# Optimization experiments

Measured on AMD Instinct MI355X. Metric: run time of the kernel, lower is better.

## Reference

```python
import jax, jax.numpy as jnp
import numpy as np

N = 100_000          # nodes
E = 3_200_000        # edges (avg degree 32)
DIMS = [6, 20, 15, 10, 5, 2]


def setup_inputs() -> dict:
    key = jax.random.key(0)
    ks = jax.random.split(key, 3 + 2 * 5)
    inp = {
        "x": jax.random.normal(ks[0], (N, DIMS[0]), jnp.float32),
        "edge_index": jax.random.randint(ks[1], (2, E), 0, N, jnp.int32),
        "edge_weight": jax.random.uniform(ks[2], (E,), jnp.float32),
    }
    for i in range(5):
        din, dout = DIMS[i], DIMS[i + 1]
        s = 1.0 / np.sqrt(din)
        inp[f"w_rel{i}"] = jax.random.normal(ks[3 + 2 * i], (din, dout), jnp.float32) * s
        inp[f"b_rel{i}"] = jnp.zeros((dout,), jnp.float32)
        inp[f"w_root{i}"] = jax.random.normal(ks[4 + 2 * i], (din, dout), jnp.float32) * s
    return inp


def _graph_conv(x, src, dst, w, W_rel, b_rel, W_root):
    # PyG GraphConv: lin_rel(scatter_add(w_e * x_src)) + lin_root(x)
    msg = x[src] * w[:, None]                                  # [E, din]
    agg = jax.ops.segment_sum(msg, dst, num_segments=N)        # [N, din]
    return agg @ W_rel + b_rel + x @ W_root                    # [N, dout]


def reference(x, edge_index, edge_weight,
              w_rel0, b_rel0, w_root0,
              w_rel1, b_rel1, w_root1,
              w_rel2, b_rel2, w_root2,
              w_rel3, b_rel3, w_root3,
              w_rel4, b_rel4, w_root4):
    src, dst = edge_index[0], edge_index[1]
    layers = [
        (w_rel0, b_rel0, w_root0),
        (w_rel1, b_rel1, w_root1),
        (w_rel2, b_rel2, w_root2),
        (w_rel3, b_rel3, w_root3),
        (w_rel4, b_rel4, w_root4),
    ]
    for W_rel, b_rel, W_root in layers:
        x = jax.nn.relu(_graph_conv(x, src, dst, edge_weight, W_rel, b_rel, W_root))
    return jax.nn.softmax(x, axis=1)
```

## Files before the change

### kernel.cpp

```cpp
#include <hip/hip_runtime.h>
#include <hip/hip_fp16.h>
#include <stdint.h>

#define N_NODES 100000
#define N_EDGES 3200000
#define BN      128
#define NB      782
#define NCH_H   1024
#define CH_H    (N_EDGES / NCH_H)
#define CPL     (NCH_H / 64)
#define PAD_PER 98
#define NCH_S   512
#define CH_S    (N_EDGES / NCH_S)
#define FPS     (NCH_H / NCH_S)
#define BS1     1024
#define S1_IT   ((CH_S + BS1 - 1) / BS1)
#define BS2     512
#define S2_CAP  4608
#define R2IT    9
#define BLOCK   256
#define W_SCALE 32767.0f
#define W_INV   (1.0f / 32767.0f)

__global__ void hist_kernel(const int* __restrict__ dst, int* __restrict__ hist_g,
                            const float* __restrict__ x, __half* __restrict__ xpad) {
    __shared__ int h[NB];
    for (int b = threadIdx.x; b < NB; b += BLOCK) h[b] = 0;
    {
        int i = blockIdx.x * PAD_PER + threadIdx.x;
        if (threadIdx.x < PAD_PER && i < N_NODES) {
            const float* xr = x + (size_t)i * 6;
            __half2 hh[4];
            hh[0] = __halves2half2(__float2half(xr[0]), __float2half(xr[1]));
            hh[1] = __halves2half2(__float2half(xr[2]), __float2half(xr[3]));
            hh[2] = __halves2half2(__float2half(xr[4]), __float2half(xr[5]));
            hh[3] = __halves2half2(__float2half(0.f),   __float2half(0.f));
            *(uint4*)(xpad + (size_t)i * 8) = *(uint4*)hh;
        }
    }
    __syncthreads();
    const int c  = blockIdx.x;
    const int k0 = c * CH_H;
    for (int k = threadIdx.x; k < CH_H; k += BLOCK)
        atomicAdd(&h[dst[k0 + k] >> 7], 1);
    __syncthreads();
    for (int b = threadIdx.x; b < NB; b += BLOCK)
        hist_g[c * NB + b] = h[b];
}

__global__ void reduce_kernel(const int* __restrict__ hist_g, int* __restrict__ tot) {
    int w    = (blockIdx.x * blockDim.x + threadIdx.x) >> 6;
    int lane = threadIdx.x & 63;
    if (w >= NB) return;
    int ls = 0;
    const int cbase = lane * CPL;
    #pragma unroll
    for (int i = 0; i < CPL; ++i) ls += hist_g[(cbase + i) * NB + w];
    #pragma unroll
    for (int d = 32; d >= 1; d >>= 1) ls += __shfl_xor(ls, d);
    if (lane == 0) tot[w] = ls;
}

#define SCAN_T   1024
__global__ void scan_kernel(const int* __restrict__ cnt, int* __restrict__ bstart,
                            int* __restrict__ gcur) {
    __shared__ int part[SCAN_T];
    int t = threadIdx.x;
    int v = (t < NB) ? cnt[t] : 0;
    part[t] = v;
    __syncthreads();
    for (int off = 1; off < SCAN_T; off <<= 1) {
        int u = (t >= off) ? part[t - off] : 0;
        __syncthreads();
        part[t] += u;
        __syncthreads();
    }
    if (t < NB) { int e = part[t] - v; bstart[t] = e; gcur[t] = e; }
}

__global__ void __launch_bounds__(BS1)
scatter1_kernel(const int* __restrict__ src, const int* __restrict__ dst,
                const float* __restrict__ w,
                int* __restrict__ gcur,
                const int* __restrict__ hist_g,
                uint2* __restrict__ rec1) {
    __shared__ uint2 stage[CH_S];
    __shared__ int h[NB];
    __shared__ int delta[NB];
    __shared__ int wtot[BS1 / 64];

    const int c  = blockIdx.x;
    const int k0 = c * CH_S;
    const int t  = threadIdx.x;

    int      dv[S1_IT];
    uint32_t sv[S1_IT];
    float    wv[S1_IT];
    #pragma unroll
    for (int i = 0; i < S1_IT; ++i) {
        int k = t + i * BS1;
        if (k < CH_S) {
            dv[i] = dst[k0 + k];
            sv[i] = (uint32_t)src[k0 + k];
            wv[i] = w[k0 + k];
        }
    }

    for (int b = t; b < NB; b += BS1) {
        int s = 0;
        #pragma unroll
        for (int f = 0; f < FPS; ++f)
            s += hist_g[(size_t)(FPS * c + f) * NB + b];
        h[b] = s;
    }
    __syncthreads();

    {
        const int base = t * 2;
        int v[2], ls = 0;
        #pragma unroll
        for (int i = 0; i < 2; ++i) {
            int idx = base + i;
            v[i] = (idx < NB) ? h[idx] : 0;
            ls += v[i];
        }
        int lane = t & 63, wvi = t >> 6;
        int run = ls;
        #pragma unroll
        for (int d = 1; d < 64; d <<= 1) {
            int u = __shfl_up(run, d);
            if (lane >= d) run += u;
        }
        if (lane == 63) wtot[wvi] = run;
        __syncthreads();
        int wexcl = 0;
        for (int i = 0; i < wvi; ++i) wexcl += wtot[i];
        int excl = wexcl + run - ls;
        #pragma unroll
        for (int i = 0; i < 2; ++i) {
            int idx = base + i;
            if (idx < NB) {
                int gb = atomicAdd(&gcur[idx], v[i]);
                h[idx]     = excl;
                delta[idx] = gb - excl;
                excl += v[i];
            }
        }
    }
    __syncthreads();

    #pragma unroll
    for (int i = 0; i < S1_IT; ++i) {
        int k = t + i * BS1;
        if (k < CH_S) {
            int d = dv[i];
            int b = d >> 7;
            int pos = atomicAdd(&h[b], 1);
            uint32_t w15 = (uint32_t)__float2uint_rn(wv[i] * W_SCALE);
            uint2 r;
            r.x = sv[i] | ((uint32_t)(d & 127) << 17);
            r.y = w15 | ((uint32_t)b << 15);
            stage[pos] = r;
        }
    }
    __syncthreads();

    #pragma unroll
    for (int i = 0; i < S1_IT; ++i) {
        int k = t + i * BS1;
        if (k < CH_S) {
            uint2 r = stage[k];
            int b = (int)(r.y >> 15);
            rec1[delta[b] + k] = r;
        }
    }
}

__global__ void __launch_bounds__(BS2)
scatter2_kernel(const uint2* __restrict__ rec1,
                const int* __restrict__ bstart, const int* __restrict__ tot,
                uint32_t* __restrict__ rec2,
                int2* __restrict__ rowcnt) {
    __shared__ int h[BN];
    __shared__ int cur[BN];
    __shared__ int wtot2[2];
    __shared__ uint32_t stage[S2_CAP];
    const int b  = blockIdx.x;
    const int s0 = bstart[b];
    const int n  = tot[b];
    const int t  = threadIdx.x;
    if (t < BN) h[t] = 0;
    __syncthreads();

    uint2 rv[R2IT];
    #pragma unroll
    for (int i = 0; i < R2IT; ++i) {
        int k = t + i * BS2;
        uint2 r = (k < n) ? rec1[s0 + k] : make_uint2(0u, 0u);
        rv[i] = r;
        if (k < n) atomicAdd(&h[r.x >> 17], 1);
    }
    for (int k = t + R2IT * BS2; k < n; k += BS2)
        atomicAdd(&h[rec1[s0 + k].x >> 17], 1);
    __syncthreads();

    int v = 0, run = 0;
    if (t < BN) {
        v = h[t];
        run = v;
        int lane = t & 63;
        #pragma unroll
        for (int d = 1; d < 64; d <<= 1) {
            int u = __shfl_up(run, d);
            if (lane >= d) run += u;
        }
        if (lane == 63) wtot2[t >> 6] = run;
    }
    __syncthreads();
    if (t < BN) {
        int excl = run - v + ((t >= 64) ? wtot2[0] : 0);
        cur[t] = excl;
        int node = b * BN + t;
        if (node < N_NODES) rowcnt[node] = make_int2(s0 + excl, v);
    }
    __syncthreads();

    #pragma unroll
    for (int i = 0; i < R2IT; ++i) {
        int k = t + i * BS2;
        if (k < n) {
            uint2 r = rv[i];
            int dl = (int)(r.x >> 17);
            uint32_t r2 = (r.x & 0x1FFFF) | ((r.y & 0x7FFF) << 17);
            int pos = atomicAdd(&cur[dl], 1);
            if (pos < S2_CAP) stage[pos] = r2;
            else              rec2[s0 + pos] = r2;
        }
    }
    for (int k = t + R2IT * BS2; k < n; k += BS2) {
        uint2 r = rec1[s0 + k];
        int dl = (int)(r.x >> 17);
        uint32_t r2 = (r.x & 0x1FFFF) | ((r.y & 0x7FFF) << 17);
        int pos = atomicAdd(&cur[dl], 1);
        if (pos < S2_CAP) stage[pos] = r2;
        else              rec2[s0 + pos] = r2;
    }
    __syncthreads();
    for (int i = t; i < n && i < S2_CAP; i += BS2)
        rec2[s0 + i] = stage[i];
}

__global__ void layer0_kernel(const __half* __restrict__ xpad,
                              const uint32_t* __restrict__ rec,
                              const int2* __restrict__ rowcnt,
                              const float* __restrict__ wrel0, const float* __restrict__ brel0,
                              const float* __restrict__ wroot0,
                              const float* __restrict__ wrel1, const float* __restrict__ brel1,
                              const float* __restrict__ wroot1,
                              __half* __restrict__ pn, float* __restrict__ oinitn) {
    __shared__ float s_wrel0[6 * 20], s_wroot0[6 * 20], s_b0[20];
    __shared__ float s_wrel1[20 * 15], s_wroot1[20 * 15], s_b1[15];
    for (int t = threadIdx.x; t < 120; t += BLOCK) {
        s_wrel0[t]  = wrel0[t];
        s_wroot0[t] = wroot0[t];
    }
    for (int t = threadIdx.x; t < 300; t += BLOCK) {
        s_wrel1[t]  = wrel1[t];
        s_wroot1[t] = wroot1[t];
    }
    if (threadIdx.x < 20) s_b0[threadIdx.x] = brel0[threadIdx.x];
    if (threadIdx.x < 15) s_b1[threadIdx.x] = brel1[threadIdx.x];
    __syncthreads();

    int t = blockIdx.x * blockDim.x + threadIdx.x;
    int node = t >> 3;
    int q    = t & 7;

    float agg[6] = {0.f, 0.f, 0.f, 0.f, 0.f, 0.f};
    const int2 rc = rowcnt[node];
    const int s = rc.x;
    const int e = rc.x + rc.y;
    for (int k = s + q; k < e; k += 32) {
        uint32_t rv[4];
        float    wv[4];
        #pragma unroll
        for (int u = 0; u < 4; ++u) {
            int kk = k + 8 * u;
            rv[u] = (kk < e) ? rec[kk] : 0u;
            wv[u] = (float)(rv[u] >> 17) * W_INV;
        }
        uint4 raw[4];
        #pragma unroll
        for (int u = 0; u < 4; ++u)
            raw[u] = *(const uint4*)(xpad + (size_t)(rv[u] & 0x1FFFF) * 8);
        #pragma unroll
        for (int u = 0; u < 4; ++u) {
            const __half2* h = (const __half2*)&raw[u];
            float w = wv[u];
            agg[0] += w * __low2float(h[0]);  agg[1] += w * __high2float(h[0]);
            agg[2] += w * __low2float(h[1]);  agg[3] += w * __high2float(h[1]);
            agg[4] += w * __low2float(h[2]);  agg[5] += w * __high2float(h[2]);
        }
    }
    #pragma unroll
    for (int i = 0; i < 6; ++i) {
        agg[i] += __shfl_xor(agg[i], 1);
        agg[i] += __shfl_xor(agg[i], 2);
        agg[i] += __shfl_xor(agg[i], 4);
    }
    uint4 raws = *(const uint4*)(xpad + (size_t)node * 8);
    const __half2* hs = (const __half2*)&raws;
    float xv[6] = { __low2float(hs[0]), __high2float(hs[0]),
                    __low2float(hs[1]), __high2float(hs[1]),
                    __low2float(hs[2]), __high2float(hs[2]) };
    float ov[20];
    #pragma unroll
    for (int j = 0; j < 20; ++j) {
        float o = s_b0[j];
        #pragma unroll
        for (int i = 0; i < 6; ++i)
            o += agg[i] * s_wrel0[i * 20 + j] + xv[i] * s_wroot0[i * 20 + j];
        ov[j] = fmaxf(o, 0.f);
    }
    {
        float pk[2] = {0.f, 0.f};
        #pragma unroll
        for (int kk = 0; kk < 2; ++kk) {
            int k = 2 * q + kk;
            if (k < 15) {
                float sacc = 0.f;
                #pragma unroll
                for (int j = 0; j < 20; ++j) sacc += ov[j] * s_wrel1[j * 15 + k];
                pk[kk] = sacc;
            }
        }
        ((__half2*)(pn + (size_t)node * 16))[q] =
            __halves2half2(__float2half(pk[0]), __float2half(pk[1]));
    }
    #pragma unroll
    for (int kk = 0; kk < 2; ++kk) {
        int k = q + kk * 8;
        if (k < 15) {
            float sacc = s_b1[k];
            #pragma unroll
            for (int j = 0; j < 20; ++j) sacc += ov[j] * s_wroot1[j * 15 + k];
            oinitn[(size_t)node * 15 + k] = sacc;
        }
    }
}

template<int DOUT, int SPH, int NDOUT, int NSPH, bool LAST>
__global__ void gather_kernel(const __half* __restrict__ p, const float* __restrict__ oinit,
                              const uint32_t* __restrict__ rec,
                              const int2* __restrict__ rowcnt,
                              const float* __restrict__ wrel_n, const float* __restrict__ brel_n,
                              const float* __restrict__ wroot_n,
                              __half* __restrict__ pn, float* __restrict__ oinitn,
                              float* __restrict__ out) {
    __shared__ float s_wrel[LAST ? 1 : DOUT * NDOUT];
    __shared__ float s_wroot[LAST ? 1 : DOUT * NDOUT];
    __shared__ float s_b[LAST ? 1 : (NDOUT > 0 ? NDOUT : 1)];
    if constexpr (!LAST) {
        for (int t = threadIdx.x; t < DOUT * NDOUT; t += BLOCK) {
            s_wrel[t]  = wrel_n[t];
            s_wroot[t] = wroot_n[t];
        }
        if (threadIdx.x < NDOUT) s_b[threadIdx.x] = brel_n[threadIdx.x];
        __syncthreads();
    }

    int t = blockIdx.x * blockDim.x + threadIdx.x;
    int node = t >> 3;
    int q    = t & 7;

    float af[SPH];
    #pragma unroll
    for (int i = 0; i < SPH; ++i) af[i] = 0.f;

    const int2 rc = rowcnt[node];
    const int s = rc.x;
    const int e = rc.x + rc.y;
    constexpr int NR = (SPH >= 8) ? SPH / 8 : 1;
    for (int k = s + q; k < e; k += 32) {
        uint32_t rv[4];
        float    wv[4];
        #pragma unroll
        for (int u = 0; u < 4; ++u) {
            int kk = k + 8 * u;
            rv[u] = (kk < e) ? rec[kk] : 0u;
            wv[u] = (float)(rv[u] >> 17) * W_INV;
        }
        if constexpr (SPH >= 8) {
            uint4 raw[4 * NR];
            #pragma unroll
            for (int u = 0; u < 4; ++u) {
                const uint4* ps = (const uint4*)(p + (size_t)(rv[u] & 0x1FFFF) * SPH);
                #pragma unroll
                for (int v = 0; v < NR; ++v) raw[u * NR + v] = ps[v];
            }
            #pragma unroll
            for (int u = 0; u < 4; ++u) {
                float w = wv[u];
                #pragma unroll
                for (int v = 0; v < NR; ++v) {
                    const __half2* h = (const __half2*)&raw[u * NR + v];
                    #pragma unroll
                    for (int jj = 0; jj < 4; ++jj) {
                        af[v * 8 + 2 * jj]     += w * __low2float(h[jj]);
                        af[v * 8 + 2 * jj + 1] += w * __high2float(h[jj]);
                    }
                }
            }
        } else {
            uint32_t raw[4];
            #pragma unroll
            for (int u = 0; u < 4; ++u)
                raw[u] = *(const uint32_t*)(p + (size_t)(rv[u] & 0x1FFFF) * SPH);
            #pragma unroll
            for (int u = 0; u < 4; ++u) {
                __half2 h = *(const __half2*)&raw[u];
                af[0] += wv[u] * __low2float(h);
                af[1] += wv[u] * __high2float(h);
            }
        }
    }
    #pragma unroll
    for (int i = 0; i < SPH; ++i) {
        af[i] += __shfl_xor(af[i], 1);
        af[i] += __shfl_xor(af[i], 2);
        af[i] += __shfl_xor(af[i], 4);
    }

    if constexpr (LAST) {
        if (q == 0) {
            float o0 = af[0] + oinit[(size_t)node * 2 + 0];
            float o1 = af[1] + oinit[(size_t)node * 2 + 1];
            float m = fmaxf(o0, o1);
            float e0 = __expf(o0 - m), e1 = __expf(o1 - m);
            float inv = 1.f / (e0 + e1);
            out[(size_t)node * 2 + 0] = e0 * inv;
            out[(size_t)node * 2 + 1] = e1 * inv;
        }
    } else {
        float ov[DOUT];
        #pragma unroll
        for (int j = 0; j < DOUT; ++j)
            ov[j] = fmaxf(af[j] + oinit[(size_t)node * DOUT + j], 0.f);

        if (q < NSPH / 2) {
            float pk[2] = {0.f, 0.f};
            #pragma unroll
            for (int kk = 0; kk < 2; ++kk) {
                int k = 2 * q + kk;
                if (k < NDOUT) {
                    float sacc = 0.f;
                    #pragma unroll
                    for (int j = 0; j < DOUT; ++j) sacc += ov[j] * s_wrel[j * NDOUT + k];
                    pk[kk] = sacc;
                }
            }
            ((__half2*)(pn + (size_t)node * NSPH))[q] =
                __halves2half2(__float2half(pk[0]), __float2half(pk[1]));
        }
        #pragma unroll
        for (int kk = 0; kk < 2; ++kk) {
            int k = q + kk * 8;
            if (k < NDOUT) {
                float sacc = s_b[k];
                #pragma unroll
                for (int j = 0; j < DOUT; ++j) sacc += ov[j] * s_wroot[j * NDOUT + k];
                oinitn[(size_t)node * NDOUT + k] = sacc;
            }
        }
    }
}


extern "C" void kernel_launch(void* const* d_in, const int* in_sizes, int n_in,
                              void* d_out, int out_size, void* d_ws, size_t ws_size,
                              hipStream_t stream) {
    const float* x  = (const float*)d_in[0];
    const int*   ei = (const int*)d_in[1];
    const float* ew = (const float*)d_in[2];
    const float* wrel[5]  = { (const float*)d_in[3], (const float*)d_in[6],
                              (const float*)d_in[9], (const float*)d_in[12],
                              (const float*)d_in[15] };
    const float* brel[5]  = { (const float*)d_in[4], (const float*)d_in[7],
                              (const float*)d_in[10], (const float*)d_in[13],
                              (const float*)d_in[16] };
    const float* wroot[5] = { (const float*)d_in[5], (const float*)d_in[8],
                              (const float*)d_in[11], (const float*)d_in[14],
                              (const float*)d_in[17] };

    char* ws = (char*)d_ws;
    size_t off = 0;
    auto alloc = [&](size_t bytes) -> void* {
        void* ptr = ws + off;
        off += (bytes + 255) & ~(size_t)255;
        return ptr;
    };
    char*     regionA   = (char*)alloc((size_t)N_EDGES * 8);
    uint2*    rec1      = (uint2*)regionA;
    __half*   pA        = (__half*)regionA;
    __half*   pB        = (__half*)(regionA + (size_t)4  * 1024 * 1024);
    float*    oA        = (float*)(regionA + (size_t)8  * 1024 * 1024);
    float*    oB        = (float*)(regionA + (size_t)16 * 1024 * 1024);
    uint32_t* rec2      = (uint32_t*)alloc((size_t)N_EDGES * 4);
    __half*   xpad      = (__half*)alloc((size_t)N_NODES * 8 * 2);
    int*      hist_g    = (int*)alloc((size_t)NCH_H * NB * 4);
    int*      tot       = (int*)alloc((size_t)NB * 4);
    int*      bstart    = (int*)alloc((size_t)NB * 4);
    int*      gcur      = (int*)alloc((size_t)NB * 4);
    int2*     rowcnt    = (int2*)alloc((size_t)N_NODES * 8);

    const int* srcv = ei;
    const int* dstv = ei + N_EDGES;

    const int gN8 = (8 * N_NODES + BLOCK - 1) / BLOCK;

    hist_kernel    <<<NCH_H, BLOCK, 0, stream>>>(dstv, hist_g, x, xpad);
    reduce_kernel  <<<(NB + 3) / 4, BLOCK, 0, stream>>>(hist_g, tot);
    scan_kernel    <<<1, SCAN_T, 0, stream>>>(tot, bstart, gcur);
    scatter1_kernel<<<NCH_S, BS1, 0, stream>>>(srcv, dstv, ew, gcur, hist_g, rec1);
    scatter2_kernel<<<NB, BS2, 0, stream>>>(rec1, bstart, tot, rec2, rowcnt);

    layer0_kernel<<<gN8, BLOCK, 0, stream>>>(xpad, rec2, rowcnt,
                                             wrel[0], brel[0], wroot[0],
                                             wrel[1], brel[1], wroot[1], pA, oA);
    gather_kernel<15, 16, 10, 16, false><<<gN8, BLOCK, 0, stream>>>(
        pA, oA, rec2, rowcnt, wrel[2], brel[2], wroot[2], pB, oB, nullptr);
    gather_kernel<10, 16, 5, 8, false><<<gN8, BLOCK, 0, stream>>>(
        pB, oB, rec2, rowcnt, wrel[3], brel[3], wroot[3], pA, oA, nullptr);
    gather_kernel<5, 8, 2, 2, false><<<gN8, BLOCK, 0, stream>>>(
        pA, oA, rec2, rowcnt, wrel[4], brel[4], wroot[4], pB, oB, nullptr);
    gather_kernel<2, 2, 0, 0, true><<<gN8, BLOCK, 0, stream>>>(
        pB, oB, rec2, rowcnt, nullptr, nullptr, nullptr,
        nullptr, nullptr, (float*)d_out);
}
```

Baseline: 282.3 us.

## Replace two-level bucket sort CSR build with per-node atomic counting sort

Builds the destination-sorted edge list with a per-node histogram using global atomics, a two-pass block scan, and a direct atomic-slot scatter. This replaces the old bucketed two-stage scatter with its shared-memory staging. Node activation buffers now get dedicated allocations instead of aliasing the old record region. The new path spreads 3.2M global atomics over 100k counters and writes scattered 4-byte records, trading extra random global traffic for fewer passes. Edge order within each row also becomes nondeterministic.

```diff
diff --git a/kernel.cpp b/kernel.cpp
--- a/kernel.cpp
+++ b/kernel.cpp
@@ -4,31 +4,26 @@
 
 #define N_NODES 100000
 #define N_EDGES 3200000
-#define BN      128
-#define NB      782
-#define NCH_H   1024
-#define CH_H    (N_EDGES / NCH_H)
-#define CPL     (NCH_H / 64)
-#define PAD_PER 98
-#define NCH_S   512
-#define CH_S    (N_EDGES / NCH_S)
-#define FPS     (NCH_H / NCH_S)
-#define BS1     1024
-#define S1_IT   ((CH_S + BS1 - 1) / BS1)
-#define BS2     512
-#define S2_CAP  4608
-#define R2IT    9
 #define BLOCK   256
+#define GN8     3125
+#define NHB     782
+#define NSB     98
 #define W_SCALE 32767.0f
 #define W_INV   (1.0f / 32767.0f)
 
-__global__ void hist_kernel(const int* __restrict__ dst, int* __restrict__ hist_g,
-                            const float* __restrict__ x, __half* __restrict__ xpad) {
-    __shared__ int h[NB];
-    for (int b = threadIdx.x; b < NB; b += BLOCK) h[b] = 0;
+__global__ void __launch_bounds__(1024)
+zero_kernel(int* __restrict__ ncnt) {
+    int i = blockIdx.x * 1024 + threadIdx.x;
+    if (i < N_NODES) ncnt[i] = 0;
+}
+
+__global__ void __launch_bounds__(1024)
+nhist_kernel(const int* __restrict__ dst, int* __restrict__ ncnt,
+             const float* __restrict__ x, __half* __restrict__ xpad) {
+    const int t = threadIdx.x, blk = blockIdx.x;
     {
-        int i = blockIdx.x * PAD_PER + threadIdx.x;
-        if (threadIdx.x < PAD_PER && i < N_NODES) {
+        int i = blk * 128 + t;
+        if (t < 128 && i < N_NODES) {
             const float* xr = x + (size_t)i * 6;
             __half2 hh[4];
             hh[0] = __halves2half2(__float2half(xr[0]), __float2half(xr[1]));
@@ -38,216 +33,84 @@
             *(uint4*)(xpad + (size_t)i * 8) = *(uint4*)hh;
         }
     }
-    __syncthreads();
-    const int c  = blockIdx.x;
-    const int k0 = c * CH_H;
-    for (int k = threadIdx.x; k < CH_H; k += BLOCK)
-        atomicAdd(&h[dst[k0 + k] >> 7], 1);
-    __syncthreads();
-    for (int b = threadIdx.x; b < NB; b += BLOCK)
-        hist_g[c * NB + b] = h[b];
-}
-
-__global__ void reduce_kernel(const int* __restrict__ hist_g, int* __restrict__ tot) {
-    int w    = (blockIdx.x * blockDim.x + threadIdx.x) >> 6;
-    int lane = threadIdx.x & 63;
-    if (w >= NB) return;
-    int ls = 0;
-    const int cbase = lane * CPL;
-    #pragma unroll
-    for (int i = 0; i < CPL; ++i) ls += hist_g[(cbase + i) * NB + w];
-    #pragma unroll
-    for (int d = 32; d >= 1; d >>= 1) ls += __shfl_xor(ls, d);
-    if (lane == 0) tot[w] = ls;
-}
-
-#define SCAN_T   1024
-__global__ void scan_kernel(const int* __restrict__ cnt, int* __restrict__ bstart,
-                            int* __restrict__ gcur) {
-    __shared__ int part[SCAN_T];
-    int t = threadIdx.x;
-    int v = (t < NB) ? cnt[t] : 0;
+    const int base = blk * 4096 + t;
+    int dv[4];
+    #pragma unroll
+    for (int u = 0; u < 4; ++u) {
+        int k = base + u * 1024;
+        dv[u] = (k < N_EDGES) ? dst[k] : -1;
+    }
+    #pragma unroll
+    for (int u = 0; u < 4; ++u)
+        if (dv[u] >= 0) atomicAdd(&ncnt[dv[u]], 1);
+}
+
+__global__ void __launch_bounds__(1024)
+partial_kernel(const int* __restrict__ ncnt, int* __restrict__ nexcl,
+               int* __restrict__ ptot) {
+    __shared__ int part[1024];
+    const int t = threadIdx.x;
+    const int idx = blockIdx.x * 1024 + t;
+    int v = (idx < N_NODES) ? ncnt[idx] : 0;
     part[t] = v;
     __syncthreads();
-    for (int off = 1; off < SCAN_T; off <<= 1) {
+    for (int off = 1; off < 1024; off <<= 1) {
         int u = (t >= off) ? part[t - off] : 0;
         __syncthreads();
         part[t] += u;
         __syncthreads();
     }
-    if (t < NB) { int e = part[t] - v; bstart[t] = e; gcur[t] = e; }
-}
-
-__global__ void __launch_bounds__(BS1)
-scatter1_kernel(const int* __restrict__ src, const int* __restrict__ dst,
-                const float* __restrict__ w,
-                int* __restrict__ gcur,
-                const int* __restrict__ hist_g,
-                uint2* __restrict__ rec1) {
-    __shared__ uint2 stage[CH_S];
-    __shared__ int h[NB];
-    __shared__ int delta[NB];
-    __shared__ int wtot[BS1 / 64];
-
-    const int c  = blockIdx.x;
-    const int k0 = c * CH_S;
-    const int t  = threadIdx.x;
-
-    int      dv[S1_IT];
-    uint32_t sv[S1_IT];
-    float    wv[S1_IT];
-    #pragma unroll
-    for (int i = 0; i < S1_IT; ++i) {
-        int k = t + i * BS1;
-        if (k < CH_S) {
-            dv[i] = dst[k0 + k];
-            sv[i] = (uint32_t)src[k0 + k];
-            wv[i] = w[k0 + k];
-        }
-    }
-
-    for (int b = t; b < NB; b += BS1) {
-        int s = 0;
-        #pragma unroll
-        for (int f = 0; f < FPS; ++f)
-            s += hist_g[(size_t)(FPS * c + f) * NB + b];
-        h[b] = s;
-    }
+    if (idx < N_NODES) nexcl[idx] = part[t] - v;
+    if (t == 1023) ptot[blockIdx.x] = part[t];
+}
+
+__global__ void __launch_bounds__(1024)
+fixup_kernel(const int* __restrict__ ncnt, const int* __restrict__ nexcl,
+             const int* __restrict__ ptot,
+             int2* __restrict__ rowcnt, int* __restrict__ ncur) {
+    __shared__ int red[1024];
+    const int t = threadIdx.x, blk = blockIdx.x;
+    red[t] = (t < blk) ? ptot[t] : 0;
     __syncthreads();
-
-    {
-        const int base = t * 2;
-        int v[2], ls = 0;
-        #pragma unroll
-        for (int i = 0; i < 2; ++i) {
-            int idx = base + i;
-            v[i] = (idx < NB) ? h[idx] : 0;
-            ls += v[i];
-        }
-        int lane = t & 63, wvi = t >> 6;
-        int run = ls;
-        #pragma unroll
-        for (int d = 1; d < 64; d <<= 1) {
-            int u = __shfl_up(run, d);
-            if (lane >= d) run += u;
-        }
-        if (lane == 63) wtot[wvi] = run;
+    for (int off = 512; off >= 1; off >>= 1) {
+        if (t < off) red[t] += red[t + off];
         __syncthreads();
-        int wexcl = 0;
-        for (int i = 0; i < wvi; ++i) wexcl += wtot[i];
-        int excl = wexcl + run - ls;
-        #pragma unroll
-        for (int i = 0; i < 2; ++i) {
-            int idx = base + i;
-            if (idx < NB) {
-                int gb = atomicAdd(&gcur[idx], v[i]);
-                h[idx]     = excl;
-                delta[idx] = gb - excl;
-                excl += v[i];
-            }
-        }
-    }
-    __syncthreads();
-
-    #pragma unroll
-    for (int i = 0; i < S1_IT; ++i) {
-        int k = t + i * BS1;
-        if (k < CH_S) {
-            int d = dv[i];
-            int b = d >> 7;
-            int pos = atomicAdd(&h[b], 1);
-            uint32_t w15 = (uint32_t)__float2uint_rn(wv[i] * W_SCALE);
-            uint2 r;
-            r.x = sv[i] | ((uint32_t)(d & 127) << 17);
-            r.y = w15 | ((uint32_t)b << 15);
-            stage[pos] = r;
-        }
-    }
-    __syncthreads();
-
-    #pragma unroll
-    for (int i = 0; i < S1_IT; ++i) {
-        int k = t + i * BS1;
-        if (k < CH_S) {
-            uint2 r = stage[k];
-            int b = (int)(r.y >> 15);
-            rec1[delta[b] + k] = r;
-        }
-    }
-}
-
-__global__ void __launch_bounds__(BS2)
-scatter2_kernel(const uint2* __restrict__ rec1,
-                const int* __restrict__ bstart, const int* __restrict__ tot,
-                uint32_t* __restrict__ rec2,
-                int2* __restrict__ rowcnt) {
-    __shared__ int h[BN];
-    __shared__ int cur[BN];
-    __shared__ int wtot2[2];
-    __shared__ uint32_t stage[S2_CAP];
-    const int b  = blockIdx.x;
-    const int s0 = bstart[b];
-    const int n  = tot[b];
-    const int t  = threadIdx.x;
-    if (t < BN) h[t] = 0;
-    __syncthreads();
-
-    uint2 rv[R2IT];
-    #pragma unroll
-    for (int i = 0; i < R2IT; ++i) {
-        int k = t + i * BS2;
-        uint2 r = (k < n) ? rec1[s0 + k] : make_uint2(0u, 0u);
-        rv[i] = r;
-        if (k < n) atomicAdd(&h[r.x >> 17], 1);
-    }
-    for (int k = t + R2IT * BS2; k < n; k += BS2)
-        atomicAdd(&h[rec1[s0 + k].x >> 17], 1);
-    __syncthreads();
-
-    int v = 0, run = 0;
-    if (t < BN) {
-        v = h[t];
-        run = v;
-        int lane = t & 63;
-        #pragma unroll
-        for (int d = 1; d < 64; d <<= 1) {
-            int u = __shfl_up(run, d);
-            if (lane >= d) run += u;
-        }
-        if (lane == 63) wtot2[t >> 6] = run;
-    }
-    __syncthreads();
-    if (t < BN) {
-        int excl = run - v + ((t >= 64) ? wtot2[0] : 0);
-        cur[t] = excl;
-        int node = b * BN + t;
-        if (node < N_NODES) rowcnt[node] = make_int2(s0 + excl, v);
-    }
-    __syncthreads();
-
-    #pragma unroll
-    for (int i = 0; i < R2IT; ++i) {
-        int k = t + i * BS2;
-        if (k < n) {
-            uint2 r = rv[i];
-            int dl = (int)(r.x >> 17);
-            uint32_t r2 = (r.x & 0x1FFFF) | ((r.y & 0x7FFF) << 17);
-            int pos = atomicAdd(&cur[dl], 1);
-            if (pos < S2_CAP) stage[pos] = r2;
-            else              rec2[s0 + pos] = r2;
-        }
-    }
-    for (int k = t + R2IT * BS2; k < n; k += BS2) {
-        uint2 r = rec1[s0 + k];
-        int dl = (int)(r.x >> 17);
-        uint32_t r2 = (r.x & 0x1FFFF) | ((r.y & 0x7FFF) << 17);
-        int pos = atomicAdd(&cur[dl], 1);
-        if (pos < S2_CAP) stage[pos] = r2;
-        else              rec2[s0 + pos] = r2;
-    }
-    __syncthreads();
-    for (int i = t; i < n && i < S2_CAP; i += BS2)
-        rec2[s0 + i] = stage[i];
+    }
+    const int base = red[0];
+    const int idx = blk * 1024 + t;
+    if (idx < N_NODES) {
+        int rs = base + nexcl[idx];
+        rowcnt[idx] = make_int2(rs, ncnt[idx]);
+        ncur[idx] = rs;
+    }
+}
+
+__global__ void __launch_bounds__(1024)
+scatter_kernel(const int* __restrict__ src, const int* __restrict__ dst,
+               const float* __restrict__ w,
+               int* __restrict__ ncur, uint32_t* __restrict__ rec2) {
+    const int t = threadIdx.x, blk = blockIdx.x;
+    const int base = blk * 4096 + t;
+    int      dv[4];
+    uint32_t sv[4];
+    float    wv[4];
+    #pragma unroll
+    for (int u = 0; u < 4; ++u) {
+        int k = base + u * 1024;
+        if (k < N_EDGES) { dv[u] = dst[k]; sv[u] = (uint32_t)src[k]; wv[u] = w[k]; }
+        else             { dv[u] = -1; sv[u] = 0u; wv[u] = 0.f; }
+    }
+    int pos[4];
+    #pragma unroll
+    for (int u = 0; u < 4; ++u)
+        pos[u] = (dv[u] >= 0) ? atomicAdd(&ncur[dv[u]], 1) : 0;
+    #pragma unroll
+    for (int u = 0; u < 4; ++u) {
+        if (dv[u] >= 0) {
+            uint32_t w15 = (uint32_t)__float2uint_rn(wv[u] * W_SCALE);
+            rec2[pos[u]] = sv[u] | (w15 << 17);
+        }
+    }
 }
 
 __global__ void layer0_kernel(const __half* __restrict__ xpad,
@@ -499,41 +362,37 @@
         off += (bytes + 255) & ~(size_t)255;
         return ptr;
     };
-    char*     regionA   = (char*)alloc((size_t)N_EDGES * 8);
-    uint2*    rec1      = (uint2*)regionA;
-    __half*   pA        = (__half*)regionA;
-    __half*   pB        = (__half*)(regionA + (size_t)4  * 1024 * 1024);
-    float*    oA        = (float*)(regionA + (size_t)8  * 1024 * 1024);
-    float*    oB        = (float*)(regionA + (size_t)16 * 1024 * 1024);
     uint32_t* rec2      = (uint32_t*)alloc((size_t)N_EDGES * 4);
+    __half*   pA        = (__half*)alloc((size_t)N_NODES * 16 * 2);
+    __half*   pB        = (__half*)alloc((size_t)N_NODES * 16 * 2);
+    float*    oA        = (float*)alloc((size_t)N_NODES * 15 * 4);
+    float*    oB        = (float*)alloc((size_t)N_NODES * 15 * 4);
     __half*   xpad      = (__half*)alloc((size_t)N_NODES * 8 * 2);
-    int*      hist_g    = (int*)alloc((size_t)NCH_H * NB * 4);
-    int*      tot       = (int*)alloc((size_t)NB * 4);
-    int*      bstart    = (int*)alloc((size_t)NB * 4);
-    int*      gcur      = (int*)alloc((size_t)NB * 4);
+    int*      ncnt      = (int*)alloc((size_t)N_NODES * 4);
+    int*      nexcl     = (int*)alloc((size_t)N_NODES * 4);
+    int*      ncur      = (int*)alloc((size_t)N_NODES * 4);
+    int*      ptot      = (int*)alloc((size_t)NSB * 4);
     int2*     rowcnt    = (int2*)alloc((size_t)N_NODES * 8);
 
     const int* srcv = ei;
     const int* dstv = ei + N_EDGES;
 
-    const int gN8 = (8 * N_NODES + BLOCK - 1) / BLOCK;
-
-    hist_kernel    <<<NCH_H, BLOCK, 0, stream>>>(dstv, hist_g, x, xpad);
-    reduce_kernel  <<<(NB + 3) / 4, BLOCK, 0, stream>>>(hist_g, tot);
-    scan_kernel    <<<1, SCAN_T, 0, stream>>>(tot, bstart, gcur);
-    scatter1_kernel<<<NCH_S, BS1, 0, stream>>>(srcv, dstv, ew, gcur, hist_g, rec1);
-    scatter2_kernel<<<NB, BS2, 0, stream>>>(rec1, bstart, tot, rec2, rowcnt);
-
-    layer0_kernel<<<gN8, BLOCK, 0, stream>>>(xpad, rec2, rowcnt,
+    zero_kernel   <<<NSB, 1024, 0, stream>>>(ncnt);
+    nhist_kernel  <<<NHB, 1024, 0, stream>>>(dstv, ncnt, x, xpad);
+    partial_kernel<<<NSB, 1024, 0, stream>>>(ncnt, nexcl, ptot);
+    fixup_kernel  <<<NSB, 1024, 0, stream>>>(ncnt, nexcl, ptot, rowcnt, ncur);
+    scatter_kernel<<<NHB, 1024, 0, stream>>>(srcv, dstv, ew, ncur, rec2);
+
+    layer0_kernel<<<GN8, BLOCK, 0, stream>>>(xpad, rec2, rowcnt,
                                              wrel[0], brel[0], wroot[0],
                                              wrel[1], brel[1], wroot[1], pA, oA);
-    gather_kernel<15, 16, 10, 16, false><<<gN8, BLOCK, 0, stream>>>(
+    gather_kernel<15, 16, 10, 16, false><<<GN8, BLOCK, 0, stream>>>(
         pA, oA, rec2, rowcnt, wrel[2], brel[2], wroot[2], pB, oB, nullptr);
-    gather_kernel<10, 16, 5, 8, false><<<gN8, BLOCK, 0, stream>>>(
+    gather_kernel<10, 16, 5, 8, false><<<GN8, BLOCK, 0, stream>>>(
         pB, oB, rec2, rowcnt, wrel[3], brel[3], wroot[3], pA, oA, nullptr);
-    gather_kernel<5, 8, 2, 2, false><<<gN8, BLOCK, 0, stream>>>(
+    gather_kernel<5, 8, 2, 2, false><<<GN8, BLOCK, 0, stream>>>(
         pA, oA, rec2, rowcnt, wrel[4], brel[4], wroot[4], pB, oB, nullptr);
-    gather_kernel<2, 2, 0, 0, true><<<gN8, BLOCK, 0, stream>>>(
+    gather_kernel<2, 2, 0, 0, true><<<GN8, BLOCK, 0, stream>>>(
         pB, oB, rec2, rowcnt, nullptr, nullptr, nullptr,
         nullptr, nullptr, (float*)d_out);
 }
```

Result: slower. 576.1 us (+104.1%).
